# Performance work log

Hardware: AMD Instinct MI355X
Metric: run time of the kernel (lower is better)

Reference implementation:

```python
import jax, jax.numpy as jnp
import numpy as np

NEG_MASK = -10000.0

def _sanitize(x):
    # torch.nan_to_num(x, nan=0.0, posinf=1.0, neginf=-1.0)
    return jnp.nan_to_num(x, nan=0.0, posinf=1.0, neginf=-1.0)

def setup_inputs() -> dict:
    key = jax.random.key(0)
    ks = jax.random.split(key, 7)
    Na, Nb, d = 4096, 4096, 256
    h = 4
    a_z = jax.random.normal(ks[0], (Na, d), dtype=jnp.float32)
    bv_z = jax.random.normal(ks[1], (Nb, d), dtype=jnp.float32)
    mask = jax.random.randint(ks[2], (Na, Nb), 0, 2) == 1
    weight = jax.random.normal(ks[3], (Na, Nb), dtype=jnp.float32)
    Wq = jax.random.normal(ks[4], (d, d), dtype=jnp.float32) * (1.0 / np.sqrt(d))
    Wk = jax.random.normal(ks[5], (d, d), dtype=jnp.float32) * (1.0 / np.sqrt(d))
    Wv = jax.random.normal(ks[6], (d, d), dtype=jnp.float32) * (1.0 / np.sqrt(d))
    return {"a_z": a_z, "bv_z": bv_z, "mask": mask, "weight": weight,
            "Wq": Wq, "Wk": Wk, "Wv": Wv, "h": h}

def reference(a_z, bv_z, mask, weight, Wq, Wk, Wv, h):
    d = a_z.shape[-1]
    dk = d // h
    # nan/inf sanitization (unconditional; identity on finite inputs, matching torch path)
    a_z = _sanitize(a_z)
    bv_z = _sanitize(bv_z)
    # projections; nn.Linear: x @ W.T. Reshape to [N, h, dk]
    q = (a_z @ Wq.T).reshape(-1, h, dk)   # [Na, h, dk]
    k = (bv_z @ Wk.T).reshape(-1, h, dk)  # [Nb, h, dk]
    v = (bv_z @ Wv.T).reshape(-1, h, dk)  # [Nb, h, dk]
    # attention scores [Na, h, Nb]
    att = jnp.einsum('ahd,bhd->ahb', q, k) / np.float32(np.sqrt(dk))
    att = jnp.where(mask[:, None, :], att, NEG_MASK)
    w = _sanitize(weight)
    att = att + w[:, None, :]
    att = jnp.clip(att, -10.0, 10.0)
    p = jax.nn.softmax(att, axis=-1)  # stable softmax (max-subtract) as in original
    # context: [Na, h, dk]; topic_align mean over heads -> [Na, dk]
    context = jnp.einsum('ahb,bhd->ahd', p, v)
    topic_align = context.mean(axis=1)
    influence = _sanitize(p.mean(axis=1).sum(axis=-1))  # [Na]
    return (topic_align, influence)
```

## Files before the change

kernel.cpp:

```cpp
#include <hip/hip_runtime.h>

#define NA 4096
#define NB 4096
#define DIM 256
#define DK 64
#define PSTR 72
#define WSTR 68
#define NSPLIT 8
#define BIT (NB / NSPLIT / 64)

typedef __attribute__((ext_vector_type(8))) short bf16x8;
typedef __attribute__((ext_vector_type(4))) float f32x4;
typedef __attribute__((ext_vector_type(4))) unsigned short us4;
typedef __attribute__((ext_vector_type(4))) int i32x4;
typedef __attribute__((ext_vector_type(2))) unsigned int u32x2;

static __device__ __forceinline__ float bf2f(unsigned short u) {
    union { unsigned int u; float f; } x;
    x.u = ((unsigned int)u) << 16;
    return x.f;
}
static __device__ __forceinline__ unsigned short f2bf(float f) {
    union { float f; unsigned int u; } x;
    x.f = f;
    unsigned int r = x.u + 0x7fffu + ((x.u >> 16) & 1u);
    return (unsigned short)(r >> 16);
}


__global__ __launch_bounds__(256) void prep_kernel(
    const float* __restrict__ a_z, const float* __restrict__ bv,
    const float* __restrict__ Wq, const float* __restrict__ Wk,
    const float* __restrict__ Wv,
    unsigned short* __restrict__ ah, unsigned short* __restrict__ al,
    unsigned short* __restrict__ bh, unsigned short* __restrict__ bl,
    unsigned short* __restrict__ wh, unsigned short* __restrict__ wl)
{
    const int idx = blockIdx.x * 256 + threadIdx.x;
    const int y = blockIdx.y;
    const float* __restrict__ src;
    unsigned short* __restrict__ dh;
    unsigned short* __restrict__ dl;
    int row, col;
    if (y == 0) {
        src = a_z; dh = ah; dl = al;
        row = (idx >> 9) * 16 + (idx & 15);
        col = ((idx >> 6) & 7) * 32 + ((idx >> 4) & 3) * 8;
    } else if (y == 1) {
        src = bv; dh = bh; dl = bl;
        row = (idx >> 9) * 16 + (idx & 15);
        col = ((idx >> 6) & 7) * 32 + ((idx >> 4) & 3) * 8;
    } else {
        if (idx >= 3 * 8192) return;
        const int m = idx >> 13;
        const int im = idx & 8191;
        src = (m == 0) ? Wq : ((m == 1) ? Wk : Wv);
        dh = wh; dl = wl;
        row = (im >> 9) * 16 + (im & 15);
        col = ((im >> 6) & 7) * 32 + ((im >> 4) & 3) * 8;
    }
    f32x4 v0 = *(const f32x4*)(src + row * DIM + col);
    f32x4 v1 = *(const f32x4*)(src + row * DIM + col + 4);
    bf16x8 h8, l8;
    #pragma unroll
    for (int r = 0; r < 4; ++r) {
        unsigned short h0 = f2bf(v0[r]);
        h8[r] = (short)h0;  l8[r] = (short)f2bf(v0[r] - bf2f(h0));
        unsigned short h1 = f2bf(v1[r]);
        h8[4 + r] = (short)h1;  l8[4 + r] = (short)f2bf(v1[r] - bf2f(h1));
    }
    *(bf16x8*)(dh + idx * 8) = h8;
    *(bf16x8*)(dl + idx * 8) = l8;
}

__global__ __launch_bounds__(256, 2) void proj_kernel(
    const unsigned short* __restrict__ ah, const unsigned short* __restrict__ al,
    const unsigned short* __restrict__ bh, const unsigned short* __restrict__ bl,
    const unsigned short* __restrict__ whc, const unsigned short* __restrict__ wlc,
    unsigned short* __restrict__ qhi, unsigned short* __restrict__ qlo,
    unsigned short* __restrict__ khi, unsigned short* __restrict__ vtout)
{
    const int mat = blockIdx.z;
    const unsigned short* __restrict__ Xh = (mat == 0) ? ah : bh;
    const unsigned short* __restrict__ Xl = (mat == 0) ? al : bl;
    const unsigned short* __restrict__ Wh = whc + mat * 65536;
    const unsigned short* __restrict__ Wl = wlc + mat * 65536;

    const int tid  = threadIdx.x;
    const int wv   = tid >> 6;
    const int lane = tid & 63;
    const int c    = lane & 15;
    const int quad = lane >> 4;
    const int n0 = blockIdx.x * 64;
    const int by = blockIdx.y;

    const unsigned short* xhp = Xh + (n0 >> 4) * 4096 + lane * 8;
    const unsigned short* xlp = Xl + (n0 >> 4) * 4096 + lane * 8;
    const unsigned short* whp = Wh + (by * 4 + wv) * 4096 + lane * 8;
    const unsigned short* wlp = Wl + (by * 4 + wv) * 4096 + lane * 8;

    f32x4 acc[4];
    #pragma unroll
    for (int nt = 0; nt < 4; ++nt) acc[nt] = (f32x4){0.f, 0.f, 0.f, 0.f};

    bf16x8 wAh, wAl, xAh[4], xAl[4];
    bf16x8 wBh, wBl, xBh[4], xBl[4];

    wAh = *(const bf16x8*)(whp);
    wAl = *(const bf16x8*)(wlp);
    #pragma unroll
    for (int nt = 0; nt < 4; ++nt) {
        xAh[nt] = *(const bf16x8*)(xhp + nt * 4096);
        xAl[nt] = *(const bf16x8*)(xlp + nt * 4096);
    }

    #pragma unroll
    for (int kk = 0; kk < 8; kk += 2) {
        wBh = *(const bf16x8*)(whp + (kk + 1) * 512);
        wBl = *(const bf16x8*)(wlp + (kk + 1) * 512);
        #pragma unroll
        for (int nt = 0; nt < 4; ++nt) {
            xBh[nt] = *(const bf16x8*)(xhp + nt * 4096 + (kk + 1) * 512);
            xBl[nt] = *(const bf16x8*)(xlp + nt * 4096 + (kk + 1) * 512);
        }
        #pragma unroll
        for (int nt = 0; nt < 4; ++nt) {
            acc[nt] = __builtin_amdgcn_mfma_f32_16x16x32_bf16(xAh[nt], wAh, acc[nt], 0, 0, 0);
            acc[nt] = __builtin_amdgcn_mfma_f32_16x16x32_bf16(xAl[nt], wAh, acc[nt], 0, 0, 0);
            acc[nt] = __builtin_amdgcn_mfma_f32_16x16x32_bf16(xAh[nt], wAl, acc[nt], 0, 0, 0);
        }
        if (kk + 2 < 8) {
            wAh = *(const bf16x8*)(whp + (kk + 2) * 512);
            wAl = *(const bf16x8*)(wlp + (kk + 2) * 512);
            #pragma unroll
            for (int nt = 0; nt < 4; ++nt) {
                xAh[nt] = *(const bf16x8*)(xhp + nt * 4096 + (kk + 2) * 512);
                xAl[nt] = *(const bf16x8*)(xlp + nt * 4096 + (kk + 2) * 512);
            }
        }
        #pragma unroll
        for (int nt = 0; nt < 4; ++nt) {
            acc[nt] = __builtin_amdgcn_mfma_f32_16x16x32_bf16(xBh[nt], wBh, acc[nt], 0, 0, 0);
            acc[nt] = __builtin_amdgcn_mfma_f32_16x16x32_bf16(xBl[nt], wBh, acc[nt], 0, 0, 0);
            acc[nt] = __builtin_amdgcn_mfma_f32_16x16x32_bf16(xBh[nt], wBl, acc[nt], 0, 0, 0);
        }
    }

    if (mat != 2) {
        const int ks = wv >> 1;
        const int lq = ((wv & 1) * 2 + (c >> 3)) * 16 + quad * 4;
        const int e  = c & 7;
        #pragma unroll
        for (int nt = 0; nt < 4; ++nt) {
            const int tbase = (((by * 256 + (n0 >> 4) + nt) * 2 + ks) * 64 + lq) * 8 + e;
            #pragma unroll
            for (int r = 0; r < 4; ++r) {
                const int idx = tbase + r * 8;
                if (mat == 0) {
                    unsigned short h = f2bf(acc[nt][r]);
                    qhi[idx] = h;
                    qlo[idx] = f2bf(acc[nt][r] - bf2f(h));
                } else {
                    khi[idx] = f2bf(acc[nt][r]);
                }
            }
        }
    } else {
        #pragma unroll
        for (int nt = 0; nt < 4; ++nt) {
            const int lv = ((nt & 1) * 2 + (quad >> 1)) * 16 + c;
            const int idx = ((((by * 64 + (n0 >> 6)) * 4 + wv) * 2 + (nt >> 1)) * 64 + lv) * 8
                            + (quad & 1) * 4;
            us4 p;
            #pragma unroll
            for (int r = 0; r < 4; ++r) p[r] = f2bf(acc[nt][r]);
            *(us4*)(vtout + idx) = p;
        }
    }
}

__global__ __launch_bounds__(256, 2) void attn_kernel(
    const unsigned short* __restrict__ qhg,
    const unsigned short* __restrict__ qlg,
    const unsigned short* __restrict__ kg,
    const unsigned short* __restrict__ vtg,
    const float* __restrict__ wg,
    const int* __restrict__ mg,
    float* __restrict__ pnum,
    float* __restrict__ pden)
{
    __shared__ float wmbuf[2][16 * WSTR];
    __shared__ unsigned short pbuf[4][16 * PSTR];

    const int tid  = threadIdx.x;
    const int wv   = tid >> 6;
    const int lane = tid & 63;
    const int c    = lane & 15;
    const int quad = lane >> 4;

    const int flat = blockIdx.y * 256 + blockIdx.x;
    const int swz  = (flat & 7) * 256 + (flat >> 3);
    const int a0   = (swz & 255) * 16;
    const int bs   = swz >> 8;
    const int bbase = bs * (NB / NSPLIT);

    const int sa = tid >> 4;
    const int sb = (tid & 15) * 4;

    unsigned kbase = (unsigned)((wv * 256 + (bbase >> 4)) * 1024 + lane * 8);
    unsigned vbase = (unsigned)((wv * 64 + (bbase >> 6)) * 4096 + lane * 8);
    const unsigned qbase = (unsigned)((wv * 256 + (a0 >> 4)) * 1024 + lane * 8);

    bf16x8 qh[2], ql[2];
    qh[0] = *(const bf16x8*)(qhg + qbase);
    qh[1] = *(const bf16x8*)(qhg + qbase + 512);
    ql[0] = *(const bf16x8*)(qlg + qbase);
    ql[1] = *(const bf16x8*)(qlg + qbase + 512);

    bf16x8 ones;
    #pragma unroll
    for (int r = 0; r < 8; ++r) ones[r] = (short)0x3F80;

    f32x4 num[4];
    #pragma unroll
    for (int nt = 0; nt < 4; ++nt) num[nt] = (f32x4){0.f, 0.f, 0.f, 0.f};
    f32x4 dacc = (f32x4){0.f, 0.f, 0.f, 0.f};

    unsigned woff = (unsigned)((a0 + sa) * NB + bbase + sb);

    {
        f32x4 w = *(const f32x4*)(wg + woff);
        i32x4 m = *(const i32x4*)(mg + woff);
        f32x4 wm;
        #pragma unroll
        for (int r = 0; r < 4; ++r) wm[r] = m[r] ? w[r] : -1.0e9f;
        *(f32x4*)(&wmbuf[0][sa * WSTR + sb]) = wm;
    }
    woff += 64;

    bf16x8 kA[4][2], kB[4][2];
    #pragma unroll
    for (int bt = 0; bt < 4; ++bt)
        #pragma unroll
        for (int ks = 0; ks < 2; ++ks)
            kA[bt][ks] = *(const bf16x8*)(kg + kbase + bt * 1024 + ks * 512);
    kbase += 4096;

#define ITER(IT, KCUR, KNXT)                                                   \
    {                                                                          \
        const int cur = (IT) & 1;                                              \
        const bool more = ((IT) + 1 < BIT);                                    \
        __syncthreads();              \
                                      \
        bf16x8 vf[4][2];                                                       \
        _Pragma("unroll")                                                      \
        for (int nt = 0; nt < 4; ++nt)                                         \
            _Pragma("unroll")                                                  \
            for (int ks2 = 0; ks2 < 2; ++ks2)                                  \
                vf[nt][ks2] = *(const bf16x8*)(vtg + vbase + nt * 1024 + ks2 * 512); \
                          \
        f32x4 wnxt; i32x4 mnxt;                                                \
        if (more) {                                                            \
            wnxt = *(const f32x4*)(wg + woff);                                 \
            mnxt = *(const i32x4*)(mg + woff);                                 \
        }                                                                      \
        __builtin_amdgcn_sched_barrier(0);                                     \
                          \
        f32x4 S[4];                                                            \
        __builtin_amdgcn_s_setprio(1);                                         \
        _Pragma("unroll")                                                      \
        for (int bt = 0; bt < 4; ++bt) {                                       \
            f32x4 s = (f32x4){0.f, 0.f, 0.f, 0.f};                             \
            s = __builtin_amdgcn_mfma_f32_16x16x32_bf16(KCUR[bt][0], qh[0], s, 0, 0, 0); \
            s = __builtin_amdgcn_mfma_f32_16x16x32_bf16(KCUR[bt][1], qh[1], s, 0, 0, 0); \
            s = __builtin_amdgcn_mfma_f32_16x16x32_bf16(KCUR[bt][0], ql[0], s, 0, 0, 0); \
            s = __builtin_amdgcn_mfma_f32_16x16x32_bf16(KCUR[bt][1], ql[1], s, 0, 0, 0); \
            S[bt] = s;                                                         \
        }                                                                      \
        __builtin_amdgcn_s_setprio(0);                                         \
                  \
        if (more) {                                                            \
            _Pragma("unroll")                                                  \
            for (int bt = 0; bt < 4; ++bt)                                     \
                _Pragma("unroll")                                              \
                for (int ks = 0; ks < 2; ++ks)                                 \
                    KNXT[bt][ks] = *(const bf16x8*)(kg + kbase + bt * 1024 + ks * 512); \
        }                                                                      \
        __builtin_amdgcn_sched_barrier(0);                                     \
        kbase += 4096; vbase += 4096; woff += 64;                              \
                                            \
        f32x4 wf[4];                                                           \
        _Pragma("unroll")                                                      \
        for (int bt = 0; bt < 4; ++bt)                                         \
            wf[bt] = *(const f32x4*)(&wmbuf[cur][c * WSTR + bt * 16 + quad * 4]); \
        \
        _Pragma("unroll")                                                      \
        for (int bt = 0; bt < 4; ++bt) {                                       \
            float ev[4];                                                       \
            _Pragma("unroll")                                                  \
            for (int r = 0; r < 4; ++r) {                                      \
                float t = fmaf(S[bt][r], 0.125f, wf[bt][r]);                   \
                t = __builtin_amdgcn_fmed3f(t, -10.0f, 10.0f);                 \
                ev[r] = exp2f(t * 1.4426950408889634f);                        \
            }                                                                  \
            unsigned p0, p1;                                                   \
            asm("v_cvt_pk_bf16_f32 %0, %1, %2" : "=v"(p0) : "v"(ev[0]), "v"(ev[1])); \
            asm("v_cvt_pk_bf16_f32 %0, %1, %2" : "=v"(p1) : "v"(ev[2]), "v"(ev[3])); \
            u32x2 pp; pp[0] = p0; pp[1] = p1;                                  \
            *(u32x2*)(&pbuf[wv][c * PSTR + bt * 16 + quad * 4]) = pp;          \
        }                                                                      \
                            \
        bf16x8 pf[2];                                                          \
        _Pragma("unroll")                                                      \
        for (int ks2 = 0; ks2 < 2; ++ks2)                                      \
            pf[ks2] = *(const bf16x8*)(&pbuf[wv][c * PSTR + ks2 * 32 + quad * 8]); \
        __builtin_amdgcn_s_setprio(1);                                         \
        _Pragma("unroll")                                                      \
        for (int nt = 0; nt < 4; ++nt) {                                       \
            num[nt] = __builtin_amdgcn_mfma_f32_16x16x32_bf16(pf[0], vf[nt][0], num[nt], 0, 0, 0); \
            num[nt] = __builtin_amdgcn_mfma_f32_16x16x32_bf16(pf[1], vf[nt][1], num[nt], 0, 0, 0); \
        }                                                                      \
        dacc = __builtin_amdgcn_mfma_f32_16x16x32_bf16(pf[0], ones, dacc, 0, 0, 0); \
        dacc = __builtin_amdgcn_mfma_f32_16x16x32_bf16(pf[1], ones, dacc, 0, 0, 0); \
        __builtin_amdgcn_s_setprio(0);                                         \
               \
        if (more) {                                                            \
            f32x4 wm;                                                          \
            _Pragma("unroll")                                                  \
            for (int r = 0; r < 4; ++r) wm[r] = mnxt[r] ? wnxt[r] : -1.0e9f;   \
            *(f32x4*)(&wmbuf[cur ^ 1][sa * WSTR + sb]) = wm;                   \
        }                                                                      \
    }

    #pragma unroll
    for (int ito = 0; ito < BIT; ito += 2) {
        ITER(ito,     kA, kB)
        ITER(ito + 1, kB, kA)
    }
#undef ITER

    const int hb = (bs * 4 + wv) * NA + a0;
    if (c == 0) {
        #pragma unroll
        for (int r = 0; r < 4; ++r)
            pden[hb + quad * 4 + r] = dacc[r];
    }

    #pragma unroll
    for (int nt = 0; nt < 4; ++nt)
        #pragma unroll
        for (int r = 0; r < 4; ++r)
            pnum[(size_t)(hb + quad * 4 + r) * DK + nt * 16 + c] = num[nt][r];
}

__global__ __launch_bounds__(256) void reduce_kernel(
    const float* __restrict__ pnum, const float* __restrict__ pden,
    float* __restrict__ outp)
{
    const int idx = blockIdx.x * 256 + threadIdx.x;
    const int a = idx >> 6, dd = idx & 63;
    float s = 0.0f;
    #pragma unroll
    for (int h = 0; h < 4; ++h) {
        float n = 0.0f, d = 0.0f;
        #pragma unroll
        for (int b = 0; b < NSPLIT; ++b) {
            n += pnum[(size_t)((b * 4 + h) * NA + a) * DK + dd];
            d += pden[(b * 4 + h) * NA + a];
        }
        s += n / d;
    }
    outp[idx] = 0.25f * s;
    if (dd == 0) outp[NA * DK + a] = 1.0f;
}

extern "C" void kernel_launch(void* const* d_in, const int* in_sizes, int n_in,
                              void* d_out, int out_size, void* d_ws, size_t ws_size,
                              hipStream_t stream) {
    const float* a_z = (const float*)d_in[0];
    const float* bv  = (const float*)d_in[1];
    const int* mask  = (const int*)d_in[2];
    const float* wgt = (const float*)d_in[3];
    const float* Wq  = (const float*)d_in[4];
    const float* Wk  = (const float*)d_in[5];
    const float* Wv  = (const float*)d_in[6];
    float* out = (float*)d_out;

    unsigned short* qhi = (unsigned short*)d_ws;
    unsigned short* qlo = qhi + NA * DIM;
    unsigned short* khi = qlo + NA * DIM;
    unsigned short* vt  = khi + NB * DIM;
    float* pnum = (float*)(vt + (size_t)DIM * NB);
    float* pden = pnum + (size_t)NSPLIT * 4 * NA * DK;
    unsigned short* ah  = (unsigned short*)pnum;
    unsigned short* al  = ah + NA * DIM;
    unsigned short* bh  = al + NA * DIM;
    unsigned short* bl  = bh + NB * DIM;
    unsigned short* whc = bl + NB * DIM;
    unsigned short* wlc = whc + 3 * 65536;

    prep_kernel<<<dim3(512, 3), 256, 0, stream>>>(a_z, bv, Wq, Wk, Wv,
                                                  ah, al, bh, bl, whc, wlc);
    proj_kernel<<<dim3(64, 4, 3), 256, 0, stream>>>(ah, al, bh, bl, whc, wlc,
                                                    qhi, qlo, khi, vt);
    attn_kernel<<<dim3(256, NSPLIT), 256, 0, stream>>>(qhi, qlo, khi, vt,
                                                       wgt, mask, pnum, pden);
    reduce_kernel<<<dim3(NA * DK / 256), 256, 0, stream>>>(pnum, pden, out);
}
```

Measured before the change: 232.3 us.

## Load weight/mask directly into MFMA fragment registers, drop LDS staging and syncthreads

Each lane now loads the weight and mask values for its own MFMA output fragment straight from global memory, replacing the cooperative LDS staging buffer and the per-iteration __syncthreads. K fragments are loaded at the start of each iteration instead of being prefetched one iteration ahead, and the outer loop is no longer force-unrolled. The packed bf16 convert asm is replaced with a software rounding f2bf. This removes block-wide sync and LDS traffic but issues four times as many smaller global loads per thread and loses K prefetch overlap, so global latency becomes more exposed.

```diff
diff --git a/kernel.cpp b/kernel.cpp
--- a/kernel.cpp
+++ b/kernel.cpp
@@ -5,7 +5,6 @@
 #define DIM 256
 #define DK 64
 #define PSTR 72
-#define WSTR 68
 #define NSPLIT 8
 #define BIT (NB / NSPLIT / 64)
 
@@ -13,7 +12,6 @@
 typedef __attribute__((ext_vector_type(4))) float f32x4;
 typedef __attribute__((ext_vector_type(4))) unsigned short us4;
 typedef __attribute__((ext_vector_type(4))) int i32x4;
-typedef __attribute__((ext_vector_type(2))) unsigned int u32x2;
 
 static __device__ __forceinline__ float bf2f(unsigned short u) {
     union { unsigned int u; float f; } x;
@@ -189,7 +187,6 @@
     float* __restrict__ pnum,
     float* __restrict__ pden)
 {
-    __shared__ float wmbuf[2][16 * WSTR];
     __shared__ unsigned short pbuf[4][16 * PSTR];
 
     const int tid  = threadIdx.x;
@@ -204,9 +201,6 @@
     const int bs   = swz >> 8;
     const int bbase = bs * (NB / NSPLIT);
 
-    const int sa = tid >> 4;
-    const int sb = (tid & 15) * 4;
-
     unsigned kbase = (unsigned)((wv * 256 + (bbase >> 4)) * 1024 + lane * 8);
     unsigned vbase = (unsigned)((wv * 64 + (bbase >> 6)) * 4096 + lane * 8);
     const unsigned qbase = (unsigned)((wv * 256 + (a0 >> 4)) * 1024 + lane * 8);
@@ -226,90 +220,75 @@
     for (int nt = 0; nt < 4; ++nt) num[nt] = (f32x4){0.f, 0.f, 0.f, 0.f};
     f32x4 dacc = (f32x4){0.f, 0.f, 0.f, 0.f};
 
-    unsigned woff = (unsigned)((a0 + sa) * NB + bbase + sb);
-
-    {
-        f32x4 w = *(const f32x4*)(wg + woff);
-        i32x4 m = *(const i32x4*)(mg + woff);
-        f32x4 wm;
-        #pragma unroll
-        for (int r = 0; r < 4; ++r) wm[r] = m[r] ? w[r] : -1.0e9f;
-        *(f32x4*)(&wmbuf[0][sa * WSTR + sb]) = wm;
-    }
-    woff += 64;
-
-    bf16x8 kA[4][2], kB[4][2];
-    #pragma unroll
-    for (int bt = 0; bt < 4; ++bt)
-        #pragma unroll
-        for (int ks = 0; ks < 2; ++ks)
-            kA[bt][ks] = *(const bf16x8*)(kg + kbase + bt * 1024 + ks * 512);
-    kbase += 4096;
-
-#define ITER(IT, KCUR, KNXT)                                                   \
+    unsigned wloff = (unsigned)((a0 + c) * NB + bbase + quad * 4);
+
+    f32x4 wfA[4], wfB[4];
+    #pragma unroll
+    for (int bt = 0; bt < 4; ++bt) {
+        f32x4 w = *(const f32x4*)(wg + wloff + bt * 16);
+        i32x4 m = *(const i32x4*)(mg + wloff + bt * 16);
+        #pragma unroll
+        for (int r = 0; r < 4; ++r) wfA[bt][r] = m[r] ? w[r] : -1.0e9f;
+    }
+    wloff += 64;
+
+#define ITER(IT, WFCUR, WFNXT)                                                 \
     {                                                                          \
-        const int cur = (IT) & 1;                                              \
         const bool more = ((IT) + 1 < BIT);                                    \
-        __syncthreads();              \
-                                      \
+                      \
+        bf16x8 kf[4][2];                                                       \
+        _Pragma("unroll")                                                      \
+        for (int bt = 0; bt < 4; ++bt)                                         \
+            _Pragma("unroll")                                                  \
+            for (int ks = 0; ks < 2; ++ks)                                     \
+                kf[bt][ks] = *(const bf16x8*)(kg + kbase + bt * 1024 + ks * 512); \
+        __builtin_amdgcn_sched_barrier(0);                                     \
+                             \
         bf16x8 vf[4][2];                                                       \
         _Pragma("unroll")                                                      \
         for (int nt = 0; nt < 4; ++nt)                                         \
             _Pragma("unroll")                                                  \
             for (int ks2 = 0; ks2 < 2; ++ks2)                                  \
                 vf[nt][ks2] = *(const bf16x8*)(vtg + vbase + nt * 1024 + ks2 * 512); \
-                          \
-        f32x4 wnxt; i32x4 mnxt;                                                \
+        __builtin_amdgcn_sched_barrier(0);                                     \
+               \
+        f32x4 wr[4]; i32x4 mr[4];                                              \
         if (more) {                                                            \
-            wnxt = *(const f32x4*)(wg + woff);                                 \
-            mnxt = *(const i32x4*)(mg + woff);                                 \
+            _Pragma("unroll")                                                  \
+            for (int bt = 0; bt < 4; ++bt) {                                   \
+                wr[bt] = *(const f32x4*)(wg + wloff + bt * 16);                \
+                mr[bt] = *(const i32x4*)(mg + wloff + bt * 16);                \
+            }                                                                  \
         }                                                                      \
         __builtin_amdgcn_sched_barrier(0);                                     \
-                          \
+        kbase += 4096; vbase += 4096; wloff += 64;                             \
+         \
         f32x4 S[4];                                                            \
         __builtin_amdgcn_s_setprio(1);                                         \
         _Pragma("unroll")                                                      \
         for (int bt = 0; bt < 4; ++bt) {                                       \
             f32x4 s = (f32x4){0.f, 0.f, 0.f, 0.f};                             \
-            s = __builtin_amdgcn_mfma_f32_16x16x32_bf16(KCUR[bt][0], qh[0], s, 0, 0, 0); \
-            s = __builtin_amdgcn_mfma_f32_16x16x32_bf16(KCUR[bt][1], qh[1], s, 0, 0, 0); \
-            s = __builtin_amdgcn_mfma_f32_16x16x32_bf16(KCUR[bt][0], ql[0], s, 0, 0, 0); \
-            s = __builtin_amdgcn_mfma_f32_16x16x32_bf16(KCUR[bt][1], ql[1], s, 0, 0, 0); \
+            s = __builtin_amdgcn_mfma_f32_16x16x32_bf16(kf[bt][0], qh[0], s, 0, 0, 0); \
+            s = __builtin_amdgcn_mfma_f32_16x16x32_bf16(kf[bt][1], qh[1], s, 0, 0, 0); \
+            s = __builtin_amdgcn_mfma_f32_16x16x32_bf16(kf[bt][0], ql[0], s, 0, 0, 0); \
+            s = __builtin_amdgcn_mfma_f32_16x16x32_bf16(kf[bt][1], ql[1], s, 0, 0, 0); \
             S[bt] = s;                                                         \
         }                                                                      \
         __builtin_amdgcn_s_setprio(0);                                         \
-                  \
-        if (more) {                                                            \
-            _Pragma("unroll")                                                  \
-            for (int bt = 0; bt < 4; ++bt)                                     \
-                _Pragma("unroll")                                              \
-                for (int ks = 0; ks < 2; ++ks)                                 \
-                    KNXT[bt][ks] = *(const bf16x8*)(kg + kbase + bt * 1024 + ks * 512); \
-        }                                                                      \
-        __builtin_amdgcn_sched_barrier(0);                                     \
-        kbase += 4096; vbase += 4096; woff += 64;                              \
-                                            \
-        f32x4 wf[4];                                                           \
-        _Pragma("unroll")                                                      \
-        for (int bt = 0; bt < 4; ++bt)                                         \
-            wf[bt] = *(const f32x4*)(&wmbuf[cur][c * WSTR + bt * 16 + quad * 4]); \
-        \
+           \
         _Pragma("unroll")                                                      \
         for (int bt = 0; bt < 4; ++bt) {                                       \
-            float ev[4];                                                       \
+            us4 p;                                                             \
             _Pragma("unroll")                                                  \
             for (int r = 0; r < 4; ++r) {                                      \
-                float t = fmaf(S[bt][r], 0.125f, wf[bt][r]);                   \
+                float t = fmaf(S[bt][r], 0.125f, WFCUR[bt][r]);                \
                 t = __builtin_amdgcn_fmed3f(t, -10.0f, 10.0f);                 \
-                ev[r] = exp2f(t * 1.4426950408889634f);                        \
+                float e = exp2f(t * 1.4426950408889634f);                      \
+                p[r] = f2bf(e);                                                \
             }                                                                  \
-            unsigned p0, p1;                                                   \
-            asm("v_cvt_pk_bf16_f32 %0, %1, %2" : "=v"(p0) : "v"(ev[0]), "v"(ev[1])); \
-            asm("v_cvt_pk_bf16_f32 %0, %1, %2" : "=v"(p1) : "v"(ev[2]), "v"(ev[3])); \
-            u32x2 pp; pp[0] = p0; pp[1] = p1;                                  \
-            *(u32x2*)(&pbuf[wv][c * PSTR + bt * 16 + quad * 4]) = pp;          \
-        }                                                                      \
-                            \
+            *(us4*)(&pbuf[wv][c * PSTR + bt * 16 + quad * 4]) = p;             \
+        }                                                                      \
+                              \
         bf16x8 pf[2];                                                          \
         _Pragma("unroll")                                                      \
         for (int ks2 = 0; ks2 < 2; ++ks2)                                      \
@@ -323,19 +302,19 @@
         dacc = __builtin_amdgcn_mfma_f32_16x16x32_bf16(pf[0], ones, dacc, 0, 0, 0); \
         dacc = __builtin_amdgcn_mfma_f32_16x16x32_bf16(pf[1], ones, dacc, 0, 0, 0); \
         __builtin_amdgcn_s_setprio(0);                                         \
-               \
+            \
         if (more) {                                                            \
-            f32x4 wm;                                                          \
-            _Pragma("unroll")                                                  \
-            for (int r = 0; r < 4; ++r) wm[r] = mnxt[r] ? wnxt[r] : -1.0e9f;   \
-            *(f32x4*)(&wmbuf[cur ^ 1][sa * WSTR + sb]) = wm;                   \
-        }                                                                      \
-    }
-
-    #pragma unroll
+            _Pragma("unroll")                                                  \
+            for (int bt = 0; bt < 4; ++bt)                                     \
+                _Pragma("unroll")                                              \
+                for (int r = 0; r < 4; ++r)                                    \
+                    WFNXT[bt][r] = mr[bt][r] ? wr[bt][r] : -1.0e9f;            \
+        }                                                                      \
+    }
+
     for (int ito = 0; ito < BIT; ito += 2) {
-        ITER(ito,     kA, kB)
-        ITER(ito + 1, kB, kA)
+        ITER(ito,     wfA, wfB)
+        ITER(ito + 1, wfB, wfA)
     }
 #undef ITER
 
```

Measured after the change: 268.9 us. +15.7%, slower.
